# Kernel tuning notes

Measured on AMD Instinct MI355X. Metric: run time of the kernel, lower is better.

## Reference

```python
import jax, jax.numpy as jnp
import numpy as np

N, D, M = 65536, 1024, 32768

def setup_inputs() -> dict:
    key = jax.random.key(0)
    k1, k2, k3, k4, k5 = jax.random.split(key, 5)
    var = jax.random.randint(k1, (N, D), -128, 128, dtype=jnp.int8)
    var_scale = jax.random.uniform(k2, (1,), jnp.float32) * 0.02 + 0.01
    indices = jax.random.randint(k3, (M, D), 0, N, dtype=jnp.int32)
    updates = (jax.random.normal(k4, (M, D)) ).astype(jnp.float16)
    smooth_scales = (jax.random.uniform(k5, (D,)) + 0.5).astype(jnp.float16)
    return {"var": var, "var_scale": var_scale, "indices": indices,
            "updates": updates, "smooth_scales": smooth_scales}

def reference(var, var_scale, indices, updates, smooth_scales):
    # dequantize int8 var with fp32 scale
    out = var.astype(jnp.float32) * var_scale  # [N, D]
    # smooth-scale the updates, promote to fp32
    upd = (updates * smooth_scales).astype(jnp.float32)  # [M, D]
    # torch scatter_add_ along axis 0: out[indices[i,j], j] += upd[i,j]
    cols = jnp.arange(out.shape[1])[None, :]  # [1, D] broadcasts vs [M, D] indices
    out = out.at[indices, cols].add(upd)
    # global abs-max -> dynamic requantization to int8
    max_val = jnp.max(jnp.abs(out))
    new_scale = max_val / 127.0
    y = jnp.clip(jnp.round(out / new_scale), -128, 127).astype(jnp.int8)
    return (y, out, new_scale[None])
```

## Files before the change

### kernel.cpp

```cpp
#include <hip/hip_runtime.h>
#include <hip/hip_fp16.h>

#define N_ROWS 65536
#define D_COLS 1024
#define M_ROWS 32768
#define HROWS  32768

using u32 = unsigned int;
using u16 = unsigned short;
typedef float f32x4 __attribute__((ext_vector_type(4)));

__global__ void init_ws_k(u32* ws) {
    if (threadIdx.x == 0 && blockIdx.x == 0) ws[0] = 0u;
}

__global__ __launch_bounds__(256) void t_idx_upd_k(const int* __restrict__ idx,
                                                   const float* __restrict__ upd,
                                                   const float* __restrict__ scl,
                                                   u16* __restrict__ idxT,
                                                   __half* __restrict__ updT) {
    __shared__ u32   sidx[64][65];
    __shared__ float supd[64][65];
    const int j0 = (int)(blockIdx.x & 15) * 64;
    const int i0 = (int)(blockIdx.x >> 4) * 64;
    const int t = threadIdx.x;

    {
        const int rr = t >> 2, c4 = t & 3;
        const int*   ip = idx + (size_t)(i0 + rr) * D_COLS + j0;
        const float* up = upd + (size_t)(i0 + rr) * D_COLS + j0;
        #pragma unroll
        for (int cq = 0; cq < 4; ++cq) {
            const int jc = cq * 16 + c4 * 4;
            const int4   iv = *(const int4*)(ip + jc);
            const float4 uv = *(const float4*)(up + jc);
            sidx[rr][jc] = (u32)iv.x; sidx[rr][jc+1] = (u32)iv.y;
            sidx[rr][jc+2] = (u32)iv.z; sidx[rr][jc+3] = (u32)iv.w;
            supd[rr][jc] = uv.x; supd[rr][jc+1] = uv.y;
            supd[rr][jc+2] = uv.z; supd[rr][jc+3] = uv.w;
        }
    }
    __syncthreads();

    {
        const int jj = t >> 2, seg = t & 3;
        const __half hs = __float2half(scl[j0 + jj]);
        u32 wi[8], wh[8];
        #pragma unroll
        for (int p = 0; p < 8; ++p) {
            const int r = seg * 16 + 2 * p;
            const u32 a = sidx[r][jj] & 0xffffu, b = sidx[r + 1][jj] & 0xffffu;
            wi[p] = a | (b << 16);
            const __half2 h2 = __halves2half2(__hmul(__float2half(supd[r][jj]), hs),
                                              __hmul(__float2half(supd[r + 1][jj]), hs));
            wh[p] = *reinterpret_cast<const u32*>(&h2);
        }
        u16* di = idxT + (size_t)(j0 + jj) * M_ROWS + i0 + seg * 16;
        __half* dh = updT + (size_t)(j0 + jj) * M_ROWS + i0 + seg * 16;
        ((uint4*)di)[0] = uint4{wi[0], wi[1], wi[2], wi[3]};
        ((uint4*)di)[1] = uint4{wi[4], wi[5], wi[6], wi[7]};
        ((uint4*)dh)[0] = uint4{wh[0], wh[1], wh[2], wh[3]};
        ((uint4*)dh)[1] = uint4{wh[4], wh[5], wh[6], wh[7]};
    }
}

__global__ __launch_bounds__(1024) void scatter_half_k(const u16* __restrict__ idxT,
                                                       const __half* __restrict__ updT,
                                                       __half* __restrict__ sumT) {
    __shared__ float acc[HROWS];
    const int bid = (blockIdx.x & 7) * 256 + (blockIdx.x >> 3);
    const int j = bid >> 1;
    const int h = bid & 1;
    const int tid = threadIdx.x;

    float4* acc4 = (float4*)acc;
    for (int t = tid; t < HROWS / 4; t += 1024) acc4[t] = float4{0.f, 0.f, 0.f, 0.f};

    const int4* ip4 = (const int4*)(idxT + (size_t)j * M_ROWS);
    const int4* up4 = (const int4*)(updT + (size_t)j * M_ROWS);
    int4 iv[4], uv[4];
    #pragma unroll
    for (int k = 0; k < 4; ++k) {
        iv[k] = ip4[k * 1024 + tid];
        uv[k] = up4[k * 1024 + tid];
    }
    __syncthreads();

    #pragma unroll
    for (int k = 0; k < 4; ++k) {
        const u32 iw[4] = {(u32)iv[k].x, (u32)iv[k].y, (u32)iv[k].z, (u32)iv[k].w};
        const u32 uw[4] = {(u32)uv[k].x, (u32)uv[k].y, (u32)uv[k].z, (u32)uv[k].w};
        #pragma unroll
        for (int e = 0; e < 4; ++e) {
            const int r0 = iw[e] & 0xffff, r1 = iw[e] >> 16;
            const __half2 h2 = *reinterpret_cast<const __half2*>(&uw[e]);
            if ((r0 >> 15) == h) atomicAdd(&acc[r0 & (HROWS - 1)], __half2float(__low2half(h2)));
            if ((r1 >> 15) == h) atomicAdd(&acc[r1 & (HROWS - 1)], __half2float(__high2half(h2)));
        }
    }
    __syncthreads();

    __half2* dst = (__half2*)(sumT + (size_t)j * N_ROWS + h * HROWS);
    for (int t = tid; t < HROWS / 2; t += 1024)
        dst[t] = __floats2half2_rn(acc[2 * t], acc[2 * t + 1]);
}

__global__ __launch_bounds__(256) void finalize_k(const int* __restrict__ var,
                                                  const __half* __restrict__ sumT,
                                                  const float* __restrict__ var_scale,
                                                  float* __restrict__ outf,
                                                  u32* __restrict__ ws) {
    __shared__ float sm[64][65];
    __shared__ float wmax[4];
    const int r0 = (int)(blockIdx.x >> 4) * 64;
    const int j0 = (int)(blockIdx.x & 15) * 64;
    const int tid = threadIdx.x;
    const float s = var_scale[0];

    {
        const int jj = tid >> 2, seg = tid & 3;
        const __half* colp = sumT + (size_t)(j0 + jj) * N_ROWS + r0 + seg * 16;
        #pragma unroll
        for (int q = 0; q < 2; ++q) {
            const uint4 w = ((const uint4*)colp)[q];
            const u32 wv[4] = {w.x, w.y, w.z, w.w};
            #pragma unroll
            for (int i = 0; i < 4; ++i) {
                const __half2 hh = *reinterpret_cast<const __half2*>(&wv[i]);
                const float2 f = __half22float2(hh);
                const int rr = seg * 16 + q * 8 + i * 2;
                sm[rr][jj] = f.x;
                sm[rr + 1][jj] = f.y;
            }
        }
    }
    __syncthreads();

    float m = 0.f;
    #pragma unroll
    for (int k = 0; k < 4; ++k) {
        const int l = k * 256 + tid;
        const int rr = l >> 4, c4 = l & 15;
        const int4 v = ((const int4*)(var + (size_t)(r0 + rr) * D_COLS + j0))[c4];
        float4 o;
        o.x = (float)v.x * s + sm[rr][c4 * 4 + 0];
        o.y = (float)v.y * s + sm[rr][c4 * 4 + 1];
        o.z = (float)v.z * s + sm[rr][c4 * 4 + 2];
        o.w = (float)v.w * s + sm[rr][c4 * 4 + 3];
        ((float4*)(outf + (size_t)(r0 + rr) * D_COLS + j0))[c4] = o;
        m = fmaxf(m, fmaxf(fmaxf(fabsf(o.x), fabsf(o.y)),
                           fmaxf(fabsf(o.z), fabsf(o.w))));
    }
    for (int off = 32; off; off >>= 1) m = fmaxf(m, __shfl_xor(m, off));
    if ((tid & 63) == 0) wmax[tid >> 6] = m;
    __syncthreads();
    if (tid == 0) {
        m = fmaxf(fmaxf(wmax[0], wmax[1]), fmaxf(wmax[2], wmax[3]));
        atomicMax(ws, __float_as_uint(m));
    }
}

__global__ __launch_bounds__(256) void quant_k(const float4* __restrict__ outf4,
                                               f32x4* __restrict__ y4,
                                               const u32* __restrict__ ws,
                                               float* __restrict__ scale_out, int n4) {
    const float mx = __uint_as_float(ws[0]);
    const float inv = 127.0f / mx;
    int gid = blockIdx.x * 256 + threadIdx.x;
    if (gid == 0) scale_out[0] = mx / 127.0f;
    const int stride = gridDim.x * 256;
    for (int i = gid; i < n4; i += stride) {
        float4 v = outf4[i];
        f32x4 o;
        o.x = fminf(fmaxf(rintf(v.x * inv), -128.f), 127.f);
        o.y = fminf(fmaxf(rintf(v.y * inv), -128.f), 127.f);
        o.z = fminf(fmaxf(rintf(v.z * inv), -128.f), 127.f);
        o.w = fminf(fmaxf(rintf(v.w * inv), -128.f), 127.f);
        __builtin_nontemporal_store(o, &y4[i]);
    }
}

extern "C" void kernel_launch(void* const* d_in, const int* in_sizes, int n_in,
                              void* d_out, int out_size, void* d_ws, size_t ws_size,
                              hipStream_t stream) {
    const int*   var       = (const int*)d_in[0];
    const float* var_scale = (const float*)d_in[1];
    const int*   idx       = (const int*)d_in[2];
    const float* upd       = (const float*)d_in[3];
    const float* scl       = (const float*)d_in[4];

    float* y    = (float*)d_out;
    float* outf = y + (size_t)N_ROWS * D_COLS;
    float* scale_out = y + 2 * (size_t)N_ROWS * D_COLS;

    char* scratch = (char*)y;
    u16*    idxT = (u16*)scratch;
    __half* updT = (__half*)(scratch + (size_t)67108864);
    __half* sumT = (__half*)(scratch + (size_t)134217728);
    u32* ws = (u32*)d_ws;

    const int n4 = N_ROWS * D_COLS / 4;

    init_ws_k<<<1, 64, 0, stream>>>(ws);
    t_idx_upd_k<<<8192, 256, 0, stream>>>(idx, upd, scl, idxT, updT);
    scatter_half_k<<<2048, 1024, 0, stream>>>(idxT, updT, sumT);
    finalize_k<<<16384, 256, 0, stream>>>(var, sumT, var_scale, outf, ws);
    quant_k<<<4096, 256, 0, stream>>>((const float4*)outf, (f32x4*)y, ws, scale_out, n4);
}
```

Measured before the change: 597.4 us.

## Split scatter into quarter-row LDS blocks and use nontemporal loads for streamed inputs

Each scatter block now covers a quarter of the output rows, using a 64KB LDS accumulator with 512 threads, so more blocks fit per CU. Each block still reads the full index and update column. The index and update loads are interleaved with the atomics instead of being preloaded. The transpose and finalize kernels read their inputs with nontemporal loads to reduce cache pollution. The cost is twice the redundant reading of the transposed index and update data in the scatter, in exchange for better occupancy.

```diff
diff --git a/kernel.cpp b/kernel.cpp
--- a/kernel.cpp
+++ b/kernel.cpp
@@ -4,11 +4,12 @@
 #define N_ROWS 65536
 #define D_COLS 1024
 #define M_ROWS 32768
-#define HROWS  32768
+#define QROWS  16384
 
 using u32 = unsigned int;
 using u16 = unsigned short;
 typedef float f32x4 __attribute__((ext_vector_type(4)));
+typedef int   i32x4 __attribute__((ext_vector_type(4)));
 
 __global__ void init_ws_k(u32* ws) {
     if (threadIdx.x == 0 && blockIdx.x == 0) ws[0] = 0u;
@@ -32,8 +33,8 @@
         #pragma unroll
         for (int cq = 0; cq < 4; ++cq) {
             const int jc = cq * 16 + c4 * 4;
-            const int4   iv = *(const int4*)(ip + jc);
-            const float4 uv = *(const float4*)(up + jc);
+            const i32x4 iv = __builtin_nontemporal_load((const i32x4*)(ip + jc));
+            const f32x4 uv = __builtin_nontemporal_load((const f32x4*)(up + jc));
             sidx[rr][jc] = (u32)iv.x; sidx[rr][jc+1] = (u32)iv.y;
             sidx[rr][jc+2] = (u32)iv.z; sidx[rr][jc+3] = (u32)iv.w;
             supd[rr][jc] = uv.x; supd[rr][jc+1] = uv.y;
@@ -64,44 +65,41 @@
     }
 }
 
-__global__ __launch_bounds__(1024) void scatter_half_k(const u16* __restrict__ idxT,
-                                                       const __half* __restrict__ updT,
-                                                       __half* __restrict__ sumT) {
-    __shared__ float acc[HROWS];
-    const int bid = (blockIdx.x & 7) * 256 + (blockIdx.x >> 3);
-    const int j = bid >> 1;
-    const int h = bid & 1;
+__global__ __launch_bounds__(512) void scatter_q_k(const u16* __restrict__ idxT,
+                                                   const __half* __restrict__ updT,
+                                                   __half* __restrict__ sumT) {
+    __shared__ float acc[QROWS];
+    const int bid = (blockIdx.x & 7) * 512 + (blockIdx.x >> 3);
+    const int j = bid >> 2;
+    const int h = bid & 3;
     const int tid = threadIdx.x;
 
     float4* acc4 = (float4*)acc;
-    for (int t = tid; t < HROWS / 4; t += 1024) acc4[t] = float4{0.f, 0.f, 0.f, 0.f};
+    for (int t = tid; t < QROWS / 4; t += 512) acc4[t] = float4{0.f, 0.f, 0.f, 0.f};
 
     const int4* ip4 = (const int4*)(idxT + (size_t)j * M_ROWS);
     const int4* up4 = (const int4*)(updT + (size_t)j * M_ROWS);
-    int4 iv[4], uv[4];
+    __syncthreads();
+
     #pragma unroll
-    for (int k = 0; k < 4; ++k) {
-        iv[k] = ip4[k * 1024 + tid];
-        uv[k] = up4[k * 1024 + tid];
-    }
-    __syncthreads();
-
-    #pragma unroll
-    for (int k = 0; k < 4; ++k) {
-        const u32 iw[4] = {(u32)iv[k].x, (u32)iv[k].y, (u32)iv[k].z, (u32)iv[k].w};
-        const u32 uw[4] = {(u32)uv[k].x, (u32)uv[k].y, (u32)uv[k].z, (u32)uv[k].w};
+    for (int k = 0; k < 8; ++k) {
+        const int t = k * 512 + tid;
+        const int4 iv = ip4[t];
+        const int4 uv = up4[t];
+        const u32 iw[4] = {(u32)iv.x, (u32)iv.y, (u32)iv.z, (u32)iv.w};
+        const u32 uw[4] = {(u32)uv.x, (u32)uv.y, (u32)uv.z, (u32)uv.w};
         #pragma unroll
         for (int e = 0; e < 4; ++e) {
             const int r0 = iw[e] & 0xffff, r1 = iw[e] >> 16;
             const __half2 h2 = *reinterpret_cast<const __half2*>(&uw[e]);
-            if ((r0 >> 15) == h) atomicAdd(&acc[r0 & (HROWS - 1)], __half2float(__low2half(h2)));
-            if ((r1 >> 15) == h) atomicAdd(&acc[r1 & (HROWS - 1)], __half2float(__high2half(h2)));
-        }
-    }
-    __syncthreads();
-
-    __half2* dst = (__half2*)(sumT + (size_t)j * N_ROWS + h * HROWS);
-    for (int t = tid; t < HROWS / 2; t += 1024)
+            if ((r0 >> 14) == h) atomicAdd(&acc[r0 & (QROWS - 1)], __half2float(__low2half(h2)));
+            if ((r1 >> 14) == h) atomicAdd(&acc[r1 & (QROWS - 1)], __half2float(__high2half(h2)));
+        }
+    }
+    __syncthreads();
+
+    __half2* dst = (__half2*)(sumT + (size_t)j * N_ROWS + h * QROWS);
+    for (int t = tid; t < QROWS / 2; t += 512)
         dst[t] = __floats2half2_rn(acc[2 * t], acc[2 * t + 1]);
 }
 
@@ -141,7 +139,8 @@
     for (int k = 0; k < 4; ++k) {
         const int l = k * 256 + tid;
         const int rr = l >> 4, c4 = l & 15;
-        const int4 v = ((const int4*)(var + (size_t)(r0 + rr) * D_COLS + j0))[c4];
+        const i32x4 v = __builtin_nontemporal_load(
+            (const i32x4*)(var + (size_t)(r0 + rr) * D_COLS + j0) + c4);
         float4 o;
         o.x = (float)v.x * s + sm[rr][c4 * 4 + 0];
         o.y = (float)v.y * s + sm[rr][c4 * 4 + 1];
@@ -203,7 +202,7 @@
 
     init_ws_k<<<1, 64, 0, stream>>>(ws);
     t_idx_upd_k<<<8192, 256, 0, stream>>>(idx, upd, scl, idxT, updT);
-    scatter_half_k<<<2048, 1024, 0, stream>>>(idxT, updT, sumT);
+    scatter_q_k<<<4096, 512, 0, stream>>>(idxT, updT, sumT);
     finalize_k<<<16384, 256, 0, stream>>>(var, sumT, var_scale, outf, ws);
     quant_k<<<4096, 256, 0, stream>>>((const float4*)outf, (f32x4*)y, ws, scale_out, n4);
 }
```

Result: faster. 574.4 us (-3.8%).
